# Kernel tuning notes

Hardware: AMD Instinct MI355X
Metric: run time of the kernel (lower is better)

Reference implementation:

```python
import jax, jax.numpy as jnp
import numpy as np

EMBED_DIM = 1024
NUM_HEADS = 16
HEAD_DIM = EMBED_DIM // NUM_HEADS
SEG_LEN = 1024  # all segment_lengths equal, dilation_rate == 1


def setup_inputs() -> dict:
    key = jax.random.key(0)
    k1, k2, k3 = jax.random.split(key, 3)
    B, S, E = 2, 4096, EMBED_DIM
    x = jax.random.normal(k1, (B, S, E), dtype=jnp.float32)
    w_qkv = jax.random.normal(k2, (3 * E, E), dtype=jnp.float32) * (E ** -0.5)
    b_qkv = jnp.zeros((3 * E,), dtype=jnp.float32)
    w_out = jax.random.normal(k3, (E, E), dtype=jnp.float32) * (E ** -0.5)
    b_out = jnp.zeros((E,), dtype=jnp.float32)
    return {"x": x, "w_qkv": w_qkv, "b_qkv": b_qkv, "w_out": w_out, "b_out": b_out}


def reference(x, w_qkv, b_qkv, w_out, b_out):
    B, S, E = x.shape
    H, Dh = NUM_HEADS, HEAD_DIM
    scale = 1.0 / np.sqrt(Dh).astype(np.float32)
    # QKV projection
    qkv = x @ w_qkv.T + b_qkv                      # [B, S, 3E]
    qkv = qkv.reshape(B, S, 3, H, Dh).transpose(2, 0, 3, 1, 4)  # [3, B, H, S, Dh]
    q, k, v = qkv[0], qkv[1], qkv[2]
    # Segments tile the sequence; each query attends only within its segment
    # (block-diagonal attention; online-softmax combine across segments is
    # trivial since the segments are disjoint in the query dimension).
    n = S // SEG_LEN
    q = q.reshape(B, H, n, SEG_LEN, Dh)
    k = k.reshape(B, H, n, SEG_LEN, Dh)
    v = v.reshape(B, H, n, SEG_LEN, Dh)
    scores = jnp.einsum("bhnqd,bhnkd->bhnqk", q, k) * scale
    attn = jax.nn.softmax(scores, axis=-1)
    out = jnp.einsum("bhnqk,bhnkd->bhnqd", attn, v)  # [B, H, n, seg, Dh]
    out = out.reshape(B, H, S, Dh).transpose(0, 2, 1, 3).reshape(B, S, E)
    return out @ w_out.T + b_out
```

## Files before the change

### kernel.cpp

```cpp
#include <hip/hip_runtime.h>

typedef __bf16 bf16x8 __attribute__((ext_vector_type(8)));
typedef float f32x4 __attribute__((ext_vector_type(4)));

#define SL2E 0.18033688011112042f

__device__ __forceinline__ unsigned short f2bf(float f) {
  union { float f; unsigned u; } v; v.f = f;
  unsigned r = v.u + 0x7fffu + ((v.u >> 16) & 1u);
  return (unsigned short)(r >> 16);
}

__device__ __forceinline__ float fast_exp2(float x) {
#if __has_builtin(__builtin_amdgcn_exp2f)
  return __builtin_amdgcn_exp2f(x);
#else
  return exp2f(x);
#endif
}

__device__ __forceinline__ unsigned pack_bf2(float lo, float hi) {
  union { float f; unsigned u; } a, b;
  a.f = lo; b.f = hi;
#if __has_builtin(__builtin_amdgcn_perm)
  return __builtin_amdgcn_perm(b.u + 0x7fffu, a.u + 0x7fffu, 0x07060302u);
#else
  return ((b.u + 0x7fffu) & 0xffff0000u) | ((a.u + 0x7fffu) >> 16);
#endif
}

__device__ __forceinline__ void gload16(const unsigned short* g, unsigned short* l) {
  __builtin_amdgcn_global_load_lds(
      (const __attribute__((address_space(1))) unsigned int*)g,
      (__attribute__((address_space(3))) unsigned int*)l, 16, 0, 0);
}

__global__ __launch_bounds__(256) void f32_to_bf16_all(
    const float* __restrict__ x, const float* __restrict__ wq, const float* __restrict__ wo,
    unsigned short* __restrict__ xb, unsigned short* __restrict__ wqb, unsigned short* __restrict__ wob) {
  int i = blockIdx.x * 256 + threadIdx.x;
  const float* src; unsigned short* dst; int off;
  if (i < 2097152) { src = x; dst = xb; off = i; }
  else if (i < 2883584) { src = wq; dst = wqb; off = i - 2097152; }
  else if (i < 3145728) { src = wo; dst = wob; off = i - 2883584; }
  else return;
  float4 v = ((const float4*)src)[off];
  ushort4 o;
  o.x = f2bf(v.x); o.y = f2bf(v.y); o.z = f2bf(v.z); o.w = f2bf(v.w);
  ((ushort4*)dst)[off] = o;
}


__global__ __launch_bounds__(256) void gemm_qkv(
    const unsigned short* __restrict__ A,
    const unsigned short* __restrict__ Bt,
    const float* __restrict__ bias,
    unsigned short* __restrict__ Qb,
    unsigned short* __restrict__ Kb,
    unsigned short* __restrict__ Vtb) {
  const int K = 1024;
  __shared__ unsigned short As[128 * 64];
  __shared__ unsigned short Bs[128 * 64];
  int tid = threadIdx.x;
  int m0 = blockIdx.x * 128, n0 = blockIdx.y * 128;
  int w = tid >> 6, lane = tid & 63, l15 = lane & 15, quad = lane >> 4;
  int wm = (w & 1) * 64, wn = (w >> 1) * 64;

  f32x4 acc[4][4] = {};

  int rs = w * 32 + (lane >> 3);
  int cs = ((lane & 7) ^ (lane >> 3)) * 8;
  const unsigned short* Ag = A + (m0 + rs) * K + cs;
  const unsigned short* Bg = Bt + (n0 + rs) * K + cs;
  unsigned short* Asl = As + w * 2048;
  unsigned short* Bsl = Bs + w * 2048;

  int t = n0 >> 10;
  int b = m0 >> 12;

  if (t != 2) {
    for (int kt = 0; kt < K; kt += 64) {
      __syncthreads();
#pragma unroll
      for (int i = 0; i < 4; ++i) {
        gload16(Ag + i * 8 * K + kt, Asl + i * 512);
        gload16(Bg + i * 8 * K + kt, Bsl + i * 512);
      }
      __syncthreads();
#pragma unroll
      for (int kk = 0; kk < 2; ++kk) {
        int swk = (((kk * 4 + quad) ^ (l15 & 7))) * 8;
        bf16x8 af[4], bfr[4];
#pragma unroll
        for (int i = 0; i < 4; ++i) af[i] = *(const bf16x8*)(As + (wm + i * 16 + l15) * 64 + swk);
#pragma unroll
        for (int j = 0; j < 4; ++j) bfr[j] = *(const bf16x8*)(Bs + (wn + j * 16 + l15) * 64 + swk);
#pragma unroll
        for (int j = 0; j < 4; ++j)
#pragma unroll
          for (int i = 0; i < 4; ++i)
            acc[j][i] = __builtin_amdgcn_mfma_f32_16x16x32_bf16(bfr[j], af[i], acc[j][i], 0, 0, 0);
      }
    }
    unsigned short* dst = (t == 0) ? Qb : Kb;
    float sc = (t == 0) ? SL2E : 1.0f;
    int h = ((n0 + wn) >> 6) & 15;
    int head_base = (b * 16 + h) * 4096 * 64;
    int s_base = (m0 & 4095) + wm;
#pragma unroll
    for (int j = 0; j < 4; ++j) {
      int d0 = j * 16 + quad * 4;
      float4 bv = *(const float4*)(bias + n0 + wn + d0);
#pragma unroll
      for (int i = 0; i < 4; ++i) {
        int s = s_base + i * 16 + l15;
        ushort4 pk;
        pk.x = f2bf((acc[j][i][0] + bv.x) * sc);
        pk.y = f2bf((acc[j][i][1] + bv.y) * sc);
        pk.z = f2bf((acc[j][i][2] + bv.z) * sc);
        pk.w = f2bf((acc[j][i][3] + bv.w) * sc);
        *(ushort4*)(dst + head_base + s * 64 + d0) = pk;
      }
    }
  } else {
    for (int kt = 0; kt < K; kt += 64) {
      __syncthreads();
#pragma unroll
      for (int i = 0; i < 4; ++i) {
        gload16(Ag + i * 8 * K + kt, Asl + i * 512);
        gload16(Bg + i * 8 * K + kt, Bsl + i * 512);
      }
      __syncthreads();
#pragma unroll
      for (int kk = 0; kk < 2; ++kk) {
        int swk = (((kk * 4 + quad) ^ (l15 & 7))) * 8;
        bf16x8 af[4], bfr[4];
#pragma unroll
        for (int i = 0; i < 4; ++i) af[i] = *(const bf16x8*)(As + (wm + i * 16 + l15) * 64 + swk);
#pragma unroll
        for (int j = 0; j < 4; ++j) bfr[j] = *(const bf16x8*)(Bs + (wn + j * 16 + l15) * 64 + swk);
#pragma unroll
        for (int i = 0; i < 4; ++i)
#pragma unroll
          for (int j = 0; j < 4; ++j)
            acc[i][j] = __builtin_amdgcn_mfma_f32_16x16x32_bf16(af[i], bfr[j], acc[i][j], 0, 0, 0);
      }
    }
    int sblk = (m0 & 4095) + wm + quad * 4;
#pragma unroll
    for (int j = 0; j < 4; ++j) {
      int n_j = n0 + wn + j * 16 + l15;
      float bv = bias[n_j];
      int h = (n_j >> 6) & 15, d = n_j & 63;
      int vbase = ((b * 16 + h) * 64 + d) * 4096;
#pragma unroll
      for (int i = 0; i < 4; ++i) {
        int s = sblk + i * 16;
        ushort4 pk;
        pk.x = f2bf(acc[i][j][0] + bv);
        pk.y = f2bf(acc[i][j][1] + bv);
        pk.z = f2bf(acc[i][j][2] + bv);
        pk.w = f2bf(acc[i][j][3] + bv);
        *(ushort4*)(Vtb + vbase + s) = pk;
      }
    }
  }
}

#define LDP 72
#define SWZ(r, cg) ((((r) * 8) + ((cg) ^ ((r) & 7))) * 8)

__global__ __launch_bounds__(256) void attn_k(
    const unsigned short* __restrict__ Qb,
    const unsigned short* __restrict__ Kb,
    const unsigned short* __restrict__ Vtb,
    unsigned short* __restrict__ Ab) {
  __shared__ unsigned short KV[2][2][4096];
  __shared__ unsigned short Ps[4][16 * LDP];

  int tid = threadIdx.x;
  int idx = blockIdx.x;
  int grp = ((idx >> 5) << 3) | (idx & 7);
  int qblk = (idx >> 3) & 3;
  int seg = grp & 3, h = (grp >> 2) & 15, b = grp >> 6;
  int w = tid >> 6, lane = tid & 63, l15 = lane & 15, quad = lane >> 4;
  int bh = b * 16 + h;
  int q0 = seg * 1024 + qblk * 256 + w * 64;

  const unsigned short* Kg = Kb + (bh * 4096 + seg * 1024) * 64;
  const unsigned short* Vg = Vtb + bh * 64 * 4096 + seg * 1024;

  int r0 = w * 16 + (lane >> 3);
  int cs = ((lane & 7) ^ (lane >> 3)) * 8;

  const unsigned short* Qg = Qb + (bh * 4096 + q0) * 64;
  bf16x8 qf[4][2];
#pragma unroll
  for (int qb = 0; qb < 4; ++qb)
#pragma unroll
    for (int kk = 0; kk < 2; ++kk)
      qf[qb][kk] = *(const bf16x8*)(Qg + (qb * 16 + l15) * 64 + kk * 32 + quad * 8);

  f32x4 o[4][4] = {};
  float lsum[4] = {0.f, 0.f, 0.f, 0.f};
  unsigned short* Pw = Ps[w];

  {
    unsigned short* dk = &KV[0][0][w * 1024];
    unsigned short* dv = &KV[0][1][w * 1024];
    gload16(Kg + r0 * 64 + cs, dk);
    gload16(Kg + (r0 + 8) * 64 + cs, dk + 512);
    gload16(Vg + r0 * 4096 + cs, dv);
    gload16(Vg + (r0 + 8) * 4096 + cs, dv + 512);
  }

#pragma unroll 2
  for (int kt = 0; kt < 16; ++kt) {
    int cur = kt & 1;
    __syncthreads();
    if (kt < 15) {
      unsigned short* dk = &KV[cur ^ 1][0][w * 1024];
      unsigned short* dv = &KV[cur ^ 1][1][w * 1024];
      const unsigned short* kN = Kg + (kt + 1) * 4096;
      const unsigned short* vN = Vg + (kt + 1) * 64;
      gload16(kN + r0 * 64 + cs, dk);
      gload16(kN + (r0 + 8) * 64 + cs, dk + 512);
      gload16(vN + r0 * 4096 + cs, dv);
      gload16(vN + (r0 + 8) * 4096 + cs, dv + 512);
    }
    const unsigned short* Kt = KV[cur][0];
    const unsigned short* Vt = KV[cur][1];

    uint2 pp[4][4];
#pragma unroll
    for (int half = 0; half < 2; ++half) {
      f32x4 st[2][4] = {};
#pragma unroll
      for (int kk = 0; kk < 2; ++kk) {
        int cg = kk * 4 + quad;
        bf16x8 kf0 = *(const bf16x8*)(Kt + SWZ(half * 32 + l15, cg));
        bf16x8 kf1 = *(const bf16x8*)(Kt + SWZ(half * 32 + 16 + l15, cg));
#pragma unroll
        for (int qb = 0; qb < 4; ++qb) {
          st[0][qb] = __builtin_amdgcn_mfma_f32_16x16x32_bf16(kf0, qf[qb][kk], st[0][qb], 0, 0, 0);
          st[1][qb] = __builtin_amdgcn_mfma_f32_16x16x32_bf16(kf1, qf[qb][kk], st[1][qb], 0, 0, 0);
        }
      }
#pragma unroll
      for (int kb = 0; kb < 2; ++kb)
#pragma unroll
        for (int qb = 0; qb < 4; ++qb) {
          f32x4 s = st[kb][qb];
          float p0 = fast_exp2(s[0]), p1 = fast_exp2(s[1]);
          float p2 = fast_exp2(s[2]), p3 = fast_exp2(s[3]);
          lsum[qb] += (p0 + p1) + (p2 + p3);
          uint2 d;
          d.x = pack_bf2(p0, p1);
          d.y = pack_bf2(p2, p3);
          pp[qb][half * 2 + kb] = d;
        }
    }

    bf16x8 vf[2][4];
#pragma unroll
    for (int kk = 0; kk < 2; ++kk)
#pragma unroll
      for (int db = 0; db < 4; ++db)
        vf[kk][db] = *(const bf16x8*)(Vt + SWZ(db * 16 + l15, kk * 4 + quad));
#pragma unroll
    for (int qb = 0; qb < 4; ++qb) {
#pragma unroll
      for (int g = 0; g < 4; ++g)
        *(uint2*)(Pw + l15 * LDP + g * 16 + quad * 4) = pp[qb][g];
#pragma unroll
      for (int kk = 0; kk < 2; ++kk) {
        bf16x8 pa = *(const bf16x8*)(Pw + l15 * LDP + kk * 32 + quad * 8);
#pragma unroll
        for (int db = 0; db < 4; ++db)
          o[qb][db] = __builtin_amdgcn_mfma_f32_16x16x32_bf16(pa, vf[kk][db], o[qb][db], 0, 0, 0);
      }
    }
  }

#pragma unroll
  for (int qb = 0; qb < 4; ++qb) {
    lsum[qb] += __shfl_xor(lsum[qb], 16);
    lsum[qb] += __shfl_xor(lsum[qb], 32);
  }

  float* Wf = (float*)(&KV[0][0][0]) + w * 1024;
#pragma unroll
  for (int qb = 0; qb < 4; ++qb) {
#pragma unroll
    for (int db = 0; db < 4; ++db)
#pragma unroll
      for (int r = 0; r < 4; ++r)
        Wf[(quad * 4 + r) * 64 + db * 16 + l15] = o[qb][db][r];
    float inv = 1.0f / lsum[qb];
    float4 x0 = *(float4*)(Wf + l15 * 64 + quad * 8);
    float4 x1 = *(float4*)(Wf + l15 * 64 + quad * 8 + 4);
    float4 x2 = *(float4*)(Wf + l15 * 64 + (quad + 4) * 8);
    float4 x3 = *(float4*)(Wf + l15 * 64 + (quad + 4) * 8 + 4);
    uint4 u0, u1;
    u0.x = pack_bf2(x0.x * inv, x0.y * inv);
    u0.y = pack_bf2(x0.z * inv, x0.w * inv);
    u0.z = pack_bf2(x1.x * inv, x1.y * inv);
    u0.w = pack_bf2(x1.z * inv, x1.w * inv);
    u1.x = pack_bf2(x2.x * inv, x2.y * inv);
    u1.y = pack_bf2(x2.z * inv, x2.w * inv);
    u1.z = pack_bf2(x3.x * inv, x3.y * inv);
    u1.w = pack_bf2(x3.z * inv, x3.w * inv);
    int sg = q0 + qb * 16 + l15;
    int base = (b * 4096 + sg) * 1024 + h * 64;
    *(uint4*)(Ab + base + quad * 8) = u0;
    *(uint4*)(Ab + base + (quad + 4) * 8) = u1;
  }
}

__global__ __launch_bounds__(256) void gemm_out(
    const unsigned short* __restrict__ A,
    const unsigned short* __restrict__ Bt,
    const float* __restrict__ bias,
    float* __restrict__ C) {
  const int K = 1024;
  __shared__ unsigned short As[128 * 64];
  __shared__ unsigned short Bs[128 * 64];
  int tid = threadIdx.x;
  int m0 = blockIdx.x * 128, n0 = blockIdx.y * 128;
  int w = tid >> 6, lane = tid & 63, l15 = lane & 15, quad = lane >> 4;
  int wm = (w & 1) * 64, wn = (w >> 1) * 64;

  f32x4 acc[4][4] = {};

  int rs = w * 32 + (lane >> 3);
  int cs = ((lane & 7) ^ (lane >> 3)) * 8;
  const unsigned short* Ag = A + (m0 + rs) * K + cs;
  const unsigned short* Bg = Bt + (n0 + rs) * K + cs;
  unsigned short* Asl = As + w * 2048;
  unsigned short* Bsl = Bs + w * 2048;

  for (int kt = 0; kt < K; kt += 64) {
    __syncthreads();
#pragma unroll
    for (int i = 0; i < 4; ++i) {
      gload16(Ag + i * 8 * K + kt, Asl + i * 512);
      gload16(Bg + i * 8 * K + kt, Bsl + i * 512);
    }
    __syncthreads();
#pragma unroll
    for (int kk = 0; kk < 2; ++kk) {
      int swk = (((kk * 4 + quad) ^ (l15 & 7))) * 8;
      bf16x8 af[4], bfr[4];
#pragma unroll
      for (int i = 0; i < 4; ++i) af[i] = *(const bf16x8*)(As + (wm + i * 16 + l15) * 64 + swk);
#pragma unroll
      for (int j = 0; j < 4; ++j) bfr[j] = *(const bf16x8*)(Bs + (wn + j * 16 + l15) * 64 + swk);
#pragma unroll
      for (int j = 0; j < 4; ++j)
#pragma unroll
        for (int i = 0; i < 4; ++i)
          acc[j][i] = __builtin_amdgcn_mfma_f32_16x16x32_bf16(bfr[j], af[i], acc[j][i], 0, 0, 0);
    }
  }

#pragma unroll
  for (int j = 0; j < 4; ++j) {
    int nb = n0 + wn + j * 16 + quad * 4;
    float4 bv = *(const float4*)(bias + nb);
#pragma unroll
    for (int i = 0; i < 4; ++i) {
      int m = m0 + wm + i * 16 + l15;
      float4 ov;
      ov.x = acc[j][i][0] + bv.x;
      ov.y = acc[j][i][1] + bv.y;
      ov.z = acc[j][i][2] + bv.z;
      ov.w = acc[j][i][3] + bv.w;
      *(float4*)(C + m * 1024 + nb) = ov;
    }
  }
}

extern "C" void kernel_launch(void* const* d_in, const int* in_sizes, int n_in,
                              void* d_out, int out_size, void* d_ws, size_t ws_size,
                              hipStream_t stream) {
  const float* x     = (const float*)d_in[0];
  const float* w_qkv = (const float*)d_in[1];
  const float* b_qkv = (const float*)d_in[2];
  const float* w_out = (const float*)d_in[3];
  const float* b_out = (const float*)d_in[4];
  float* out = (float*)d_out;
  char* ws = (char*)d_ws;

  unsigned short* wqkvb = (unsigned short*)(ws);
  unsigned short* woutb = (unsigned short*)(ws + 6291456);
  unsigned short* Qb    = (unsigned short*)(ws + 8388608);
  unsigned short* Kb    = (unsigned short*)(ws + 25165824);
  unsigned short* Vtb   = (unsigned short*)(ws + 41943040);
  unsigned short* xb    = (unsigned short*)(ws + 58720256);
  unsigned short* Ab    = xb;

  f32_to_bf16_all<<<12288, 256, 0, stream>>>(x, w_qkv, w_out, xb, wqkvb, woutb);
  gemm_qkv<<<dim3(64, 24), 256, 0, stream>>>(xb, wqkvb, b_qkv, Qb, Kb, Vtb);
  attn_k<<<512, 256, 0, stream>>>(Qb, Kb, Vtb, Ab);
  gemm_out<<<dim3(64, 8), 256, 0, stream>>>(Ab, woutb, b_out, out);
}
```

Baseline: 234.5 us.

## Rewrite QKV GEMM as 256x256 tile with double-buffered LDS pipeline

The QKV projection GEMM moves from 128x128 tiles with 4 waves to 256x256 tiles with 8 waves. Global-to-LDS loads are double-buffered, so the next K tile is fetched while the current one feeds MFMA. MFMA work is split into quadrants separated by barriers, with setprio raised around the math, and block IDs are remapped for locality. The goal is to hide load latency and raise arithmetic intensity, at the cost of more registers, 128KB of LDS, and fewer, larger blocks that could leave CUs underused.

```diff
diff --git a/kernel.cpp b/kernel.cpp
--- a/kernel.cpp
+++ b/kernel.cpp
@@ -34,6 +34,8 @@
       (const __attribute__((address_space(1))) unsigned int*)g,
       (__attribute__((address_space(3))) unsigned int*)l, 16, 0, 0);
 }
+
+#define SWZ(r, cg) ((((r) * 8) + ((cg) ^ ((r) & 7))) * 8)
 
 __global__ __launch_bounds__(256) void f32_to_bf16_all(
     const float* __restrict__ x, const float* __restrict__ wq, const float* __restrict__ wo,
@@ -51,7 +53,103 @@
 }
 
 
-__global__ __launch_bounds__(256) void gemm_qkv(
+template <bool SWAP>
+__device__ __forceinline__ void mfma_quad(f32x4 acc[8][4], const bf16x8 af[4][2],
+                                          const bf16x8 bn[4][2], int ibase, int jbase) {
+#pragma unroll
+  for (int kk = 0; kk < 2; ++kk)
+#pragma unroll
+    for (int i = 0; i < 4; ++i)
+#pragma unroll
+      for (int j = 0; j < 2; ++j) {
+        if constexpr (SWAP)
+          acc[ibase + i][jbase + j] = __builtin_amdgcn_mfma_f32_16x16x32_bf16(
+              bn[jbase + j][kk], af[i][kk], acc[ibase + i][jbase + j], 0, 0, 0);
+        else
+          acc[ibase + i][jbase + j] = __builtin_amdgcn_mfma_f32_16x16x32_bf16(
+              af[i][kk], bn[jbase + j][kk], acc[ibase + i][jbase + j], 0, 0, 0);
+      }
+}
+
+template <bool SWAP>
+__device__ __forceinline__ void ktile(
+    const unsigned short* Ar, const unsigned short* Br,
+    const unsigned short* AgN, const unsigned short* BgN,
+    unsigned short* Aw, unsigned short* Bw,
+    bool do_stage, int w, int l15, int quad, int wm, int wn,
+    f32x4 acc[8][4]) {
+  const int K = 1024;
+  asm volatile("s_waitcnt vmcnt(0)" ::: "memory");
+  __builtin_amdgcn_s_barrier();
+  bf16x8 af[4][2], bn[4][2];
+#pragma unroll
+  for (int kk = 0; kk < 2; ++kk) {
+#pragma unroll
+    for (int i = 0; i < 4; ++i)
+      af[i][kk] = *(const bf16x8*)(Ar + SWZ(wm + i * 16 + l15, kk * 4 + quad));
+#pragma unroll
+    for (int j = 0; j < 2; ++j)
+      bn[j][kk] = *(const bf16x8*)(Br + SWZ(wn + j * 16 + l15, kk * 4 + quad));
+  }
+  if (do_stage) {
+#pragma unroll
+    for (int i = 0; i < 4; ++i) {
+      gload16(AgN + i * 8 * K, Aw + w * 2048 + i * 512);
+      gload16(BgN + i * 8 * K, Bw + w * 2048 + i * 512);
+    }
+  }
+  __builtin_amdgcn_s_barrier();
+  asm volatile("s_waitcnt lgkmcnt(0)" ::: "memory");
+  __builtin_amdgcn_sched_barrier(0);
+  __builtin_amdgcn_s_setprio(1);
+  mfma_quad<SWAP>(acc, af, bn, 0, 0);
+  __builtin_amdgcn_s_setprio(0);
+  __builtin_amdgcn_s_barrier();
+#pragma unroll
+  for (int kk = 0; kk < 2; ++kk)
+#pragma unroll
+    for (int j = 2; j < 4; ++j)
+      bn[j][kk] = *(const bf16x8*)(Br + SWZ(wn + j * 16 + l15, kk * 4 + quad));
+  __builtin_amdgcn_s_barrier();
+  asm volatile("s_waitcnt lgkmcnt(0)" ::: "memory");
+  __builtin_amdgcn_sched_barrier(0);
+  __builtin_amdgcn_s_setprio(1);
+  mfma_quad<SWAP>(acc, af, bn, 0, 2);
+  __builtin_amdgcn_s_setprio(0);
+  __builtin_amdgcn_s_barrier();
+#pragma unroll
+  for (int kk = 0; kk < 2; ++kk)
+#pragma unroll
+    for (int i = 0; i < 4; ++i)
+      af[i][kk] = *(const bf16x8*)(Ar + SWZ(wm + (i + 4) * 16 + l15, kk * 4 + quad));
+  __builtin_amdgcn_s_barrier();
+  asm volatile("s_waitcnt lgkmcnt(0)" ::: "memory");
+  __builtin_amdgcn_sched_barrier(0);
+  __builtin_amdgcn_s_setprio(1);
+  mfma_quad<SWAP>(acc, af, bn, 4, 0);
+  __builtin_amdgcn_s_setprio(0);
+  __builtin_amdgcn_s_barrier();
+  __builtin_amdgcn_s_setprio(1);
+  mfma_quad<SWAP>(acc, af, bn, 4, 2);
+  __builtin_amdgcn_s_setprio(0);
+  __builtin_amdgcn_s_barrier();
+}
+
+template <bool SWAP>
+__device__ __forceinline__ void mainloop256(
+    const unsigned short* Ag, const unsigned short* Bg,
+    unsigned short* A0, unsigned short* B0, unsigned short* A1, unsigned short* B1,
+    int w, int l15, int quad, int wm, int wn, f32x4 acc[8][4]) {
+#pragma unroll 1
+  for (int kt2 = 0; kt2 < 16; kt2 += 2) {
+    ktile<SWAP>(A0, B0, Ag + (kt2 + 1) * 64, Bg + (kt2 + 1) * 64, A1, B1,
+                true, w, l15, quad, wm, wn, acc);
+    ktile<SWAP>(A1, B1, Ag + (kt2 + 2) * 64, Bg + (kt2 + 2) * 64, A0, B0,
+                kt2 < 14, w, l15, quad, wm, wn, acc);
+  }
+}
+
+__global__ __launch_bounds__(512, 2) void gemm_qkv(
     const unsigned short* __restrict__ A,
     const unsigned short* __restrict__ Bt,
     const float* __restrict__ bias,
@@ -59,49 +157,34 @@
     unsigned short* __restrict__ Kb,
     unsigned short* __restrict__ Vtb) {
   const int K = 1024;
-  __shared__ unsigned short As[128 * 64];
-  __shared__ unsigned short Bs[128 * 64];
+  __shared__ unsigned short As[2][16384];
+  __shared__ unsigned short Bs[2][16384];
   int tid = threadIdx.x;
-  int m0 = blockIdx.x * 128, n0 = blockIdx.y * 128;
   int w = tid >> 6, lane = tid & 63, l15 = lane & 15, quad = lane >> 4;
-  int wm = (w & 1) * 64, wn = (w >> 1) * 64;
-
-  f32x4 acc[4][4] = {};
+  int lid = blockIdx.x;
+  int nlid = (lid & 7) * 48 + (lid >> 3);
+  int m0 = (nlid & 31) * 256, n0 = (nlid >> 5) * 256;
+  int wr = w >> 2, wm = wr * 128, wn = (w & 3) * 64;
+
+  f32x4 acc[8][4] = {};
 
   int rs = w * 32 + (lane >> 3);
   int cs = ((lane & 7) ^ (lane >> 3)) * 8;
   const unsigned short* Ag = A + (m0 + rs) * K + cs;
   const unsigned short* Bg = Bt + (n0 + rs) * K + cs;
-  unsigned short* Asl = As + w * 2048;
-  unsigned short* Bsl = Bs + w * 2048;
 
   int t = n0 >> 10;
   int b = m0 >> 12;
 
+#pragma unroll
+  for (int i = 0; i < 4; ++i) {
+    gload16(Ag + i * 8 * K, &As[0][0] + w * 2048 + i * 512);
+    gload16(Bg + i * 8 * K, &Bs[0][0] + w * 2048 + i * 512);
+  }
+
   if (t != 2) {
-    for (int kt = 0; kt < K; kt += 64) {
-      __syncthreads();
-#pragma unroll
-      for (int i = 0; i < 4; ++i) {
-        gload16(Ag + i * 8 * K + kt, Asl + i * 512);
-        gload16(Bg + i * 8 * K + kt, Bsl + i * 512);
-      }
-      __syncthreads();
-#pragma unroll
-      for (int kk = 0; kk < 2; ++kk) {
-        int swk = (((kk * 4 + quad) ^ (l15 & 7))) * 8;
-        bf16x8 af[4], bfr[4];
-#pragma unroll
-        for (int i = 0; i < 4; ++i) af[i] = *(const bf16x8*)(As + (wm + i * 16 + l15) * 64 + swk);
-#pragma unroll
-        for (int j = 0; j < 4; ++j) bfr[j] = *(const bf16x8*)(Bs + (wn + j * 16 + l15) * 64 + swk);
-#pragma unroll
-        for (int j = 0; j < 4; ++j)
-#pragma unroll
-          for (int i = 0; i < 4; ++i)
-            acc[j][i] = __builtin_amdgcn_mfma_f32_16x16x32_bf16(bfr[j], af[i], acc[j][i], 0, 0, 0);
-      }
-    }
+    mainloop256<true>(Ag, Bg, &As[0][0], &Bs[0][0], &As[1][0], &Bs[1][0],
+                      w, l15, quad, wm, wn, acc);
     unsigned short* dst = (t == 0) ? Qb : Kb;
     float sc = (t == 0) ? SL2E : 1.0f;
     int h = ((n0 + wn) >> 6) & 15;
@@ -112,49 +195,28 @@
       int d0 = j * 16 + quad * 4;
       float4 bv = *(const float4*)(bias + n0 + wn + d0);
 #pragma unroll
-      for (int i = 0; i < 4; ++i) {
+      for (int i = 0; i < 8; ++i) {
         int s = s_base + i * 16 + l15;
         ushort4 pk;
-        pk.x = f2bf((acc[j][i][0] + bv.x) * sc);
-        pk.y = f2bf((acc[j][i][1] + bv.y) * sc);
-        pk.z = f2bf((acc[j][i][2] + bv.z) * sc);
-        pk.w = f2bf((acc[j][i][3] + bv.w) * sc);
+        pk.x = f2bf((acc[i][j][0] + bv.x) * sc);
+        pk.y = f2bf((acc[i][j][1] + bv.y) * sc);
+        pk.z = f2bf((acc[i][j][2] + bv.z) * sc);
+        pk.w = f2bf((acc[i][j][3] + bv.w) * sc);
         *(ushort4*)(dst + head_base + s * 64 + d0) = pk;
       }
     }
   } else {
-    for (int kt = 0; kt < K; kt += 64) {
-      __syncthreads();
-#pragma unroll
-      for (int i = 0; i < 4; ++i) {
-        gload16(Ag + i * 8 * K + kt, Asl + i * 512);
-        gload16(Bg + i * 8 * K + kt, Bsl + i * 512);
-      }
-      __syncthreads();
-#pragma unroll
-      for (int kk = 0; kk < 2; ++kk) {
-        int swk = (((kk * 4 + quad) ^ (l15 & 7))) * 8;
-        bf16x8 af[4], bfr[4];
-#pragma unroll
-        for (int i = 0; i < 4; ++i) af[i] = *(const bf16x8*)(As + (wm + i * 16 + l15) * 64 + swk);
-#pragma unroll
-        for (int j = 0; j < 4; ++j) bfr[j] = *(const bf16x8*)(Bs + (wn + j * 16 + l15) * 64 + swk);
-#pragma unroll
-        for (int i = 0; i < 4; ++i)
-#pragma unroll
-          for (int j = 0; j < 4; ++j)
-            acc[i][j] = __builtin_amdgcn_mfma_f32_16x16x32_bf16(af[i], bfr[j], acc[i][j], 0, 0, 0);
-      }
-    }
+    mainloop256<false>(Ag, Bg, &As[0][0], &Bs[0][0], &As[1][0], &Bs[1][0],
+                       w, l15, quad, wm, wn, acc);
     int sblk = (m0 & 4095) + wm + quad * 4;
 #pragma unroll
     for (int j = 0; j < 4; ++j) {
       int n_j = n0 + wn + j * 16 + l15;
       float bv = bias[n_j];
-      int h = (n_j >> 6) & 15, d = n_j & 63;
-      int vbase = ((b * 16 + h) * 64 + d) * 4096;
-#pragma unroll
-      for (int i = 0; i < 4; ++i) {
+      int hh = (n_j >> 6) & 15, d = n_j & 63;
+      int vbase = ((b * 16 + hh) * 64 + d) * 4096;
+#pragma unroll
+      for (int i = 0; i < 8; ++i) {
         int s = sblk + i * 16;
         ushort4 pk;
         pk.x = f2bf(acc[i][j][0] + bv);
@@ -168,7 +230,6 @@
 }
 
 #define LDP 72
-#define SWZ(r, cg) ((((r) * 8) + ((cg) ^ ((r) & 7))) * 8)
 
 __global__ __launch_bounds__(256) void attn_k(
     const unsigned short* __restrict__ Qb,
@@ -323,8 +384,8 @@
     const float* __restrict__ bias,
     float* __restrict__ C) {
   const int K = 1024;
-  __shared__ unsigned short As[128 * 64];
-  __shared__ unsigned short Bs[128 * 64];
+  __shared__ unsigned short As2[128 * 64];
+  __shared__ unsigned short Bs2[128 * 64];
   int tid = threadIdx.x;
   int m0 = blockIdx.x * 128, n0 = blockIdx.y * 128;
   int w = tid >> 6, lane = tid & 63, l15 = lane & 15, quad = lane >> 4;
@@ -336,8 +397,8 @@
   int cs = ((lane & 7) ^ (lane >> 3)) * 8;
   const unsigned short* Ag = A + (m0 + rs) * K + cs;
   const unsigned short* Bg = Bt + (n0 + rs) * K + cs;
-  unsigned short* Asl = As + w * 2048;
-  unsigned short* Bsl = Bs + w * 2048;
+  unsigned short* Asl = As2 + w * 2048;
+  unsigned short* Bsl = Bs2 + w * 2048;
 
   for (int kt = 0; kt < K; kt += 64) {
     __syncthreads();
@@ -352,9 +413,9 @@
       int swk = (((kk * 4 + quad) ^ (l15 & 7))) * 8;
       bf16x8 af[4], bfr[4];
 #pragma unroll
-      for (int i = 0; i < 4; ++i) af[i] = *(const bf16x8*)(As + (wm + i * 16 + l15) * 64 + swk);
-#pragma unroll
-      for (int j = 0; j < 4; ++j) bfr[j] = *(const bf16x8*)(Bs + (wn + j * 16 + l15) * 64 + swk);
+      for (int i = 0; i < 4; ++i) af[i] = *(const bf16x8*)(As2 + (wm + i * 16 + l15) * 64 + swk);
+#pragma unroll
+      for (int j = 0; j < 4; ++j) bfr[j] = *(const bf16x8*)(Bs2 + (wn + j * 16 + l15) * 64 + swk);
 #pragma unroll
       for (int j = 0; j < 4; ++j)
 #pragma unroll
@@ -400,7 +461,7 @@
   unsigned short* Ab    = xb;
 
   f32_to_bf16_all<<<12288, 256, 0, stream>>>(x, w_qkv, w_out, xb, wqkvb, woutb);
-  gemm_qkv<<<dim3(64, 24), 256, 0, stream>>>(xb, wqkvb, b_qkv, Qb, Kb, Vtb);
+  gemm_qkv<<<384, 512, 0, stream>>>(xb, wqkvb, b_qkv, Qb, Kb, Vtb);
   attn_k<<<512, 256, 0, stream>>>(Qb, Kb, Vtb, Ab);
   gemm_out<<<dim3(64, 8), 256, 0, stream>>>(Ab, woutb, b_out, out);
 }
```

After: 255.3 us. 8.9% more time.

## Double-buffer LDS tiles in QKV GEMM to overlap global loads with MFMA

Applied to the files above, without the earlier changes.

Replaces the single-buffered load-sync-compute loop in the QKV projection GEMM with a two-stage ping-pong LDS pipeline. The next K tile is fetched with global_load_lds while the current one feeds the MFMAs, using explicit vmcnt waits and raw s_barrier in place of two __syncthreads per iteration. The aim is to hide global memory latency behind compute. It doubles LDS use per block (64KB), which may lower occupancy, and it relies on hand-counted vmcnt values being correct.

```diff
diff --git a/kernel.cpp b/kernel.cpp
--- a/kernel.cpp
+++ b/kernel.cpp
@@ -34,6 +34,8 @@
       (const __attribute__((address_space(1))) unsigned int*)g,
       (__attribute__((address_space(3))) unsigned int*)l, 16, 0, 0);
 }
+
+#define SWZ(r, cg) ((((r) * 8) + ((cg) ^ ((r) & 7))) * 8)
 
 __global__ __launch_bounds__(256) void f32_to_bf16_all(
     const float* __restrict__ x, const float* __restrict__ wq, const float* __restrict__ wo,
@@ -51,6 +53,77 @@
 }
 
 
+template <bool SWAP>
+__device__ __forceinline__ void qkv_tile_compute(
+    const unsigned short* Acur, const unsigned short* Bcur,
+    int l15, int quad, int wm, int wn, f32x4 acc[4][4]) {
+#pragma unroll
+  for (int kk = 0; kk < 2; ++kk) {
+    int swk = (((kk * 4 + quad) ^ (l15 & 7))) * 8;
+    bf16x8 af[4], bfr[4];
+#pragma unroll
+    for (int i = 0; i < 4; ++i) af[i] = *(const bf16x8*)(Acur + (wm + i * 16 + l15) * 64 + swk);
+#pragma unroll
+    for (int j = 0; j < 4; ++j) bfr[j] = *(const bf16x8*)(Bcur + (wn + j * 16 + l15) * 64 + swk);
+    if constexpr (SWAP) {
+#pragma unroll
+      for (int j = 0; j < 4; ++j)
+#pragma unroll
+        for (int i = 0; i < 4; ++i)
+          acc[j][i] = __builtin_amdgcn_mfma_f32_16x16x32_bf16(bfr[j], af[i], acc[j][i], 0, 0, 0);
+    } else {
+#pragma unroll
+      for (int i = 0; i < 4; ++i)
+#pragma unroll
+        for (int j = 0; j < 4; ++j)
+          acc[i][j] = __builtin_amdgcn_mfma_f32_16x16x32_bf16(af[i], bfr[j], acc[i][j], 0, 0, 0);
+    }
+  }
+}
+
+template <bool SWAP>
+__device__ __forceinline__ void gemm_mainloop_dbuf(
+    const unsigned short* Ag, const unsigned short* Bg,
+    unsigned short* A0, unsigned short* B0,
+    unsigned short* A1, unsigned short* B1,
+    int w, int l15, int quad, int wm, int wn, f32x4 acc[4][4]) {
+  const int K = 1024;
+  unsigned short* Aw[2] = {A0 + w * 2048, A1 + w * 2048};
+  unsigned short* Bw[2] = {B0 + w * 2048, B1 + w * 2048};
+#pragma unroll
+  for (int i = 0; i < 4; ++i) {
+    gload16(Ag + i * 8 * K, Aw[0] + i * 512);
+    gload16(Bg + i * 8 * K, Bw[0] + i * 512);
+  }
+#pragma unroll 1
+  for (int kt2 = 0; kt2 < 16; kt2 += 2) {
+#pragma unroll
+    for (int i = 0; i < 4; ++i) {
+      gload16(Ag + i * 8 * K + (kt2 + 1) * 64, Aw[1] + i * 512);
+      gload16(Bg + i * 8 * K + (kt2 + 1) * 64, Bw[1] + i * 512);
+    }
+    asm volatile("s_waitcnt vmcnt(8)" ::: "memory");
+    __builtin_amdgcn_s_barrier();
+    __builtin_amdgcn_sched_barrier(0);
+    qkv_tile_compute<SWAP>(A0, B0, l15, quad, wm, wn, acc);
+    __builtin_amdgcn_s_barrier();
+    if (kt2 < 14) {
+#pragma unroll
+      for (int i = 0; i < 4; ++i) {
+        gload16(Ag + i * 8 * K + (kt2 + 2) * 64, Aw[0] + i * 512);
+        gload16(Bg + i * 8 * K + (kt2 + 2) * 64, Bw[0] + i * 512);
+      }
+      asm volatile("s_waitcnt vmcnt(8)" ::: "memory");
+    } else {
+      asm volatile("s_waitcnt vmcnt(0)" ::: "memory");
+    }
+    __builtin_amdgcn_s_barrier();
+    __builtin_amdgcn_sched_barrier(0);
+    qkv_tile_compute<SWAP>(A1, B1, l15, quad, wm, wn, acc);
+    __builtin_amdgcn_s_barrier();
+  }
+}
+
 __global__ __launch_bounds__(256) void gemm_qkv(
     const unsigned short* __restrict__ A,
     const unsigned short* __restrict__ Bt,
@@ -59,8 +132,8 @@
     unsigned short* __restrict__ Kb,
     unsigned short* __restrict__ Vtb) {
   const int K = 1024;
-  __shared__ unsigned short As[128 * 64];
-  __shared__ unsigned short Bs[128 * 64];
+  __shared__ unsigned short As[2][8192];
+  __shared__ unsigned short Bs[2][8192];
   int tid = threadIdx.x;
   int m0 = blockIdx.x * 128, n0 = blockIdx.y * 128;
   int w = tid >> 6, lane = tid & 63, l15 = lane & 15, quad = lane >> 4;
@@ -72,36 +145,13 @@
   int cs = ((lane & 7) ^ (lane >> 3)) * 8;
   const unsigned short* Ag = A + (m0 + rs) * K + cs;
   const unsigned short* Bg = Bt + (n0 + rs) * K + cs;
-  unsigned short* Asl = As + w * 2048;
-  unsigned short* Bsl = Bs + w * 2048;
 
   int t = n0 >> 10;
   int b = m0 >> 12;
 
   if (t != 2) {
-    for (int kt = 0; kt < K; kt += 64) {
-      __syncthreads();
-#pragma unroll
-      for (int i = 0; i < 4; ++i) {
-        gload16(Ag + i * 8 * K + kt, Asl + i * 512);
-        gload16(Bg + i * 8 * K + kt, Bsl + i * 512);
-      }
-      __syncthreads();
-#pragma unroll
-      for (int kk = 0; kk < 2; ++kk) {
-        int swk = (((kk * 4 + quad) ^ (l15 & 7))) * 8;
-        bf16x8 af[4], bfr[4];
-#pragma unroll
-        for (int i = 0; i < 4; ++i) af[i] = *(const bf16x8*)(As + (wm + i * 16 + l15) * 64 + swk);
-#pragma unroll
-        for (int j = 0; j < 4; ++j) bfr[j] = *(const bf16x8*)(Bs + (wn + j * 16 + l15) * 64 + swk);
-#pragma unroll
-        for (int j = 0; j < 4; ++j)
-#pragma unroll
-          for (int i = 0; i < 4; ++i)
-            acc[j][i] = __builtin_amdgcn_mfma_f32_16x16x32_bf16(bfr[j], af[i], acc[j][i], 0, 0, 0);
-      }
-    }
+    gemm_mainloop_dbuf<true>(Ag, Bg, &As[0][0], &Bs[0][0], &As[1][0], &Bs[1][0],
+                             w, l15, quad, wm, wn, acc);
     unsigned short* dst = (t == 0) ? Qb : Kb;
     float sc = (t == 0) ? SL2E : 1.0f;
     int h = ((n0 + wn) >> 6) & 15;
@@ -123,29 +173,8 @@
       }
     }
   } else {
-    for (int kt = 0; kt < K; kt += 64) {
-      __syncthreads();
-#pragma unroll
-      for (int i = 0; i < 4; ++i) {
-        gload16(Ag + i * 8 * K + kt, Asl + i * 512);
-        gload16(Bg + i * 8 * K + kt, Bsl + i * 512);
-      }
-      __syncthreads();
-#pragma unroll
-      for (int kk = 0; kk < 2; ++kk) {
-        int swk = (((kk * 4 + quad) ^ (l15 & 7))) * 8;
-        bf16x8 af[4], bfr[4];
-#pragma unroll
-        for (int i = 0; i < 4; ++i) af[i] = *(const bf16x8*)(As + (wm + i * 16 + l15) * 64 + swk);
-#pragma unroll
-        for (int j = 0; j < 4; ++j) bfr[j] = *(const bf16x8*)(Bs + (wn + j * 16 + l15) * 64 + swk);
-#pragma unroll
-        for (int i = 0; i < 4; ++i)
-#pragma unroll
-          for (int j = 0; j < 4; ++j)
-            acc[i][j] = __builtin_amdgcn_mfma_f32_16x16x32_bf16(af[i], bfr[j], acc[i][j], 0, 0, 0);
-      }
-    }
+    gemm_mainloop_dbuf<false>(Ag, Bg, &As[0][0], &Bs[0][0], &As[1][0], &Bs[1][0],
+                              w, l15, quad, wm, wn, acc);
     int sblk = (m0 & 4095) + wm + quad * 4;
 #pragma unroll
     for (int j = 0; j < 4; ++j) {
@@ -168,7 +197,6 @@
 }
 
 #define LDP 72
-#define SWZ(r, cg) ((((r) * 8) + ((cg) ^ ((r) & 7))) * 8)
 
 __global__ __launch_bounds__(256) void attn_k(
     const unsigned short* __restrict__ Qb,
@@ -323,8 +351,8 @@
     const float* __restrict__ bias,
     float* __restrict__ C) {
   const int K = 1024;
-  __shared__ unsigned short As[128 * 64];
-  __shared__ unsigned short Bs[128 * 64];
+  __shared__ unsigned short As2[128 * 64];
+  __shared__ unsigned short Bs2[128 * 64];
   int tid = threadIdx.x;
   int m0 = blockIdx.x * 128, n0 = blockIdx.y * 128;
   int w = tid >> 6, lane = tid & 63, l15 = lane & 15, quad = lane >> 4;
@@ -336,8 +364,8 @@
   int cs = ((lane & 7) ^ (lane >> 3)) * 8;
   const unsigned short* Ag = A + (m0 + rs) * K + cs;
   const unsigned short* Bg = Bt + (n0 + rs) * K + cs;
-  unsigned short* Asl = As + w * 2048;
-  unsigned short* Bsl = Bs + w * 2048;
+  unsigned short* Asl = As2 + w * 2048;
+  unsigned short* Bsl = Bs2 + w * 2048;
 
   for (int kt = 0; kt < K; kt += 64) {
     __syncthreads();
@@ -352,9 +380,9 @@
       int swk = (((kk * 4 + quad) ^ (l15 & 7))) * 8;
       bf16x8 af[4], bfr[4];
 #pragma unroll
-      for (int i = 0; i < 4; ++i) af[i] = *(const bf16x8*)(As + (wm + i * 16 + l15) * 64 + swk);
-#pragma unroll
-      for (int j = 0; j < 4; ++j) bfr[j] = *(const bf16x8*)(Bs + (wn + j * 16 + l15) * 64 + swk);
+      for (int i = 0; i < 4; ++i) af[i] = *(const bf16x8*)(As2 + (wm + i * 16 + l15) * 64 + swk);
+#pragma unroll
+      for (int j = 0; j < 4; ++j) bfr[j] = *(const bf16x8*)(Bs2 + (wn + j * 16 + l15) * 64 + swk);
 #pragma unroll
       for (int j = 0; j < 4; ++j)
 #pragma unroll
```

Result: slower. 239.5 us (+2.1%).
